# Performance work log

Hardware: AMD Instinct MI355X
Metric: run time of the kernel (lower is better)

## Reference

```python
import jax, jax.numpy as jnp
import numpy as np

N_NODES = 50000
IN_CH = 128
OUT_CH = 64
N_EDGES = 800000
K_HOPS = 2


def setup_inputs() -> dict:
    key = jax.random.key(0)
    k1, k2, k3, k4 = jax.random.split(key, 4)
    x = jax.random.normal(k1, (N_NODES, IN_CH), dtype=jnp.float32)
    edge_index = jax.random.randint(k2, (2, N_EDGES), 0, N_NODES, dtype=jnp.int64)
    # SGC linear layer params (torch Linear default init approx)
    scale = 1.0 / np.sqrt(IN_CH)
    W = jax.random.uniform(k3, (IN_CH, OUT_CH), dtype=jnp.float32, minval=-scale, maxval=scale)
    b = jax.random.uniform(k4, (OUT_CH,), dtype=jnp.float32, minval=-scale, maxval=scale)
    return {"x": x, "edge_index": edge_index, "W": W, "b": b}


def _sgc_propagate(x, row, col, K):
    # GCN symmetric normalization with self-loops: S = D^-1/2 (A+I) D^-1/2
    n = x.shape[0]
    loop = jnp.arange(n, dtype=row.dtype)
    row = jnp.concatenate([row, loop])
    col = jnp.concatenate([col, loop])
    ones = jnp.ones(row.shape[0], dtype=x.dtype)
    deg = jax.ops.segment_sum(ones, col, num_segments=n)
    dinv = jnp.where(deg > 0, jax.lax.rsqrt(deg), 0.0)
    norm = dinv[row] * dinv[col]  # [E+N]
    for _ in range(K):
        # gather source features, weight, scatter-add to targets
        msg = norm[:, None] * x[row]  # [E+N, C]
        x = jax.ops.segment_sum(msg, col, num_segments=n)
    return x


def reference(x, edge_index, W, b):
    # Dropout is identity in eval mode (deterministic reference).
    row, col = edge_index[0], edge_index[1]
    h = _sgc_propagate(x, row, col, K_HOPS)  # [N, IN_CH]
    return h @ W + b  # [N, OUT_CH]
```

## Files before the change

kernel.cpp:

```cpp
#include <hip/hip_runtime.h>

#define N_NODES 50000
#define IN_CH   128
#define OUT_CH  64
#define N_EDGES 800000
#define CAP     96
#define SCAT_B  242
#define GEMM_B  782


__device__ __forceinline__ unsigned int bpack(float a, float b) {
    unsigned int ua = __float_as_uint(a), ub = __float_as_uint(b);
    unsigned int ra = (ua + 0x7fffu + ((ua >> 16) & 1u)) >> 16;
    unsigned int rb = (ub + 0x7fffu + ((ub >> 16) & 1u)) & 0xffff0000u;
    return (ra & 0xffffu) | rb;
}


__global__ __launch_bounds__(256) void gemm_scatter(const float* __restrict__ x,
        const float* __restrict__ W, const int* __restrict__ row,
        const int* __restrict__ col, float* __restrict__ y,
        int* __restrict__ fill, unsigned short* __restrict__ esrc) {
    const int bid = blockIdx.x, tid = threadIdx.x;
    if (bid < SCAT_B) {
        for (int e = bid * 256 + tid; e < N_EDGES; e += SCAT_B * 256) {
            int s = row[e], t = col[e];
            int pos = atomicAdd(&fill[t], 1);
            if (pos < CAP) esrc[pos * N_NODES + t] = (unsigned short)s;
        }
        return;
    }
    __shared__ float sW[IN_CH * OUT_CH];
    {
        const float4* W4 = (const float4*)W;
        float4* sW4 = (float4*)sW;
        #pragma unroll
        for (int i = 0; i < 8; ++i) sW4[tid + i * 256] = W4[tid + i * 256];
    }

    const int q   = tid & 7;
    const int seg = tid >> 3;
    const int n0  = (bid - SCAT_B) * 64;
    const int na  = n0 + seg;
    const int nb  = n0 + 32 + seg;
    const int ca  = (na < N_NODES) ? na : N_NODES - 1;
    const int cb  = (nb < N_NODES) ? nb : N_NODES - 1;

    float xa[16], xb[16];
    {
        const float4* ra = (const float4*)(x + (size_t)ca * IN_CH + q * 16);
        const float4* rb = (const float4*)(x + (size_t)cb * IN_CH + q * 16);
        #pragma unroll
        for (int j = 0; j < 4; ++j) {
            ((float4*)xa)[j] = ra[j];
            ((float4*)xb)[j] = rb[j];
        }
    }
    __syncthreads();

    float acca[8] = {}, accb[8] = {};
    for (int k0 = 0; k0 < 8; ++k0) {
        #pragma unroll
        for (int i = 0; i < 16; ++i) {
            float ka = __shfl(xa[i], k0, 8);
            float kb = __shfl(xb[i], k0, 8);
            const float* wr = &sW[((k0 * 16 + i) << 6) + q * 8];
            float4 w0 = *(const float4*)wr;
            float4 w1 = *(const float4*)(wr + 4);
            acca[0] += ka * w0.x; acca[1] += ka * w0.y;
            acca[2] += ka * w0.z; acca[3] += ka * w0.w;
            acca[4] += ka * w1.x; acca[5] += ka * w1.y;
            acca[6] += ka * w1.z; acca[7] += ka * w1.w;
            accb[0] += kb * w0.x; accb[1] += kb * w0.y;
            accb[2] += kb * w0.z; accb[3] += kb * w0.w;
            accb[4] += kb * w1.x; accb[5] += kb * w1.y;
            accb[6] += kb * w1.z; accb[7] += kb * w1.w;
        }
    }
    if (na < N_NODES) {
        *(float4*)(y + (size_t)na * OUT_CH + q * 8) =
            make_float4(acca[0], acca[1], acca[2], acca[3]);
        *(float4*)(y + (size_t)na * OUT_CH + q * 8 + 4) =
            make_float4(acca[4], acca[5], acca[6], acca[7]);
    }
    if (nb < N_NODES) {
        *(float4*)(y + (size_t)nb * OUT_CH + q * 8) =
            make_float4(accb[0], accb[1], accb[2], accb[3]);
        *(float4*)(y + (size_t)nb * OUT_CH + q * 8 + 4) =
            make_float4(accb[4], accb[5], accb[6], accb[7]);
    }
}


__global__ __launch_bounds__(256) void scale_z0(const float* __restrict__ y,
        const int* __restrict__ fill, uint4* __restrict__ z0) {
    int gid = blockIdx.x * 256 + threadIdx.x;
    if (gid >= N_NODES * 8) return;
    int n = gid >> 3, q = gid & 7;
    int deg = fill[n]; if (deg > CAP) deg = CAP;
    float d = rsqrtf((float)(deg + 1));
    float4 a = ((const float4*)y)[n * 16 + q * 2];
    float4 b = ((const float4*)y)[n * 16 + q * 2 + 1];
    uint4 pk;
    pk.x = bpack(d * a.x, d * a.y);
    pk.y = bpack(d * a.z, d * a.w);
    pk.z = bpack(d * b.x, d * b.y);
    pk.w = bpack(d * b.z, d * b.w);
    z0[gid] = pk;
}


__global__ __launch_bounds__(256) void hop_gather(const uint4* __restrict__ hin,
        void* __restrict__ hout, const int* __restrict__ fill,
        const unsigned short* __restrict__ esrc, const float* __restrict__ bias,
        int last) {
    int lane = threadIdx.x & 63;
    int g = lane >> 3;
    int q = lane & 7;
    int t = __builtin_amdgcn_readfirstlane(blockIdx.x * 4 + (threadIdx.x >> 6));
    if (t >= N_NODES) return;
    int deg = fill[t]; if (deg > CAP) deg = CAP;

    float acc[8] = {};
    if (g == 0) {
        uint4 r = hin[t * 8 + q];
        const unsigned int rw[4] = { r.x, r.y, r.z, r.w };
        #pragma unroll
        for (int j = 0; j < 4; ++j) {
            acc[2 * j]     = __uint_as_float(rw[j] << 16);
            acc[2 * j + 1] = __uint_as_float(rw[j] & 0xffff0000u);
        }
    }
    for (int base = 0; base < deg; base += 8) {
        int e = base + g;
        if (e < deg) {
            int s = (int)esrc[(size_t)e * N_NODES + t];
            uint4 r = hin[s * 8 + q];
            const unsigned int rw[4] = { r.x, r.y, r.z, r.w };
            #pragma unroll
            for (int j = 0; j < 4; ++j) {
                acc[2 * j]     += __uint_as_float(rw[j] << 16);
                acc[2 * j + 1] += __uint_as_float(rw[j] & 0xffff0000u);
            }
        }
    }
    #pragma unroll
    for (int j = 0; j < 8; ++j) {
        acc[j] += __shfl_xor(acc[j], 8);
        acc[j] += __shfl_xor(acc[j], 16);
        acc[j] += __shfl_xor(acc[j], 32);
    }
    if (g == 0) {
        if (!last) {
            float rdeg = 1.0f / (float)(deg + 1);
            uint4 pk;
            pk.x = bpack(acc[0] * rdeg, acc[1] * rdeg);
            pk.y = bpack(acc[2] * rdeg, acc[3] * rdeg);
            pk.z = bpack(acc[4] * rdeg, acc[5] * rdeg);
            pk.w = bpack(acc[6] * rdeg, acc[7] * rdeg);
            ((uint4*)hout)[t * 8 + q] = pk;
        } else {
            float d = rsqrtf((float)(deg + 1));
            float4 b0 = ((const float4*)bias)[q * 2];
            float4 b1 = ((const float4*)bias)[q * 2 + 1];
            float4 o0 = make_float4(d * acc[0] + b0.x, d * acc[1] + b0.y,
                                    d * acc[2] + b0.z, d * acc[3] + b0.w);
            float4 o1 = make_float4(d * acc[4] + b1.x, d * acc[5] + b1.y,
                                    d * acc[6] + b1.z, d * acc[7] + b1.w);
            ((float4*)hout)[t * 16 + q * 2]     = o0;
            ((float4*)hout)[t * 16 + q * 2 + 1] = o1;
        }
    }
}


extern "C" void kernel_launch(void* const* d_in, const int* in_sizes, int n_in,
                              void* d_out, int out_size, void* d_ws, size_t ws_size,
                              hipStream_t stream) {
    const float* x  = (const float*)d_in[0];
    const int*   ei = (const int*)d_in[1];
    const float* W  = (const float*)d_in[2];
    const float* b  = (const float*)d_in[3];
    float*       out = (float*)d_out;

    const int* row = ei;
    const int* col = ei + N_EDGES;

    char* ws = (char*)d_ws;
    size_t a = 0;
    auto alloc = [&](size_t bytes) { char* p = ws + a; a = (a + bytes + 255) & ~(size_t)255; return p; };
    int*            fill = (int*)            alloc(N_NODES * sizeof(int));
    unsigned short* esrc = (unsigned short*) alloc((size_t)CAP * N_NODES * sizeof(unsigned short));
    float*          y    = (float*)          alloc((size_t)N_NODES * OUT_CH * sizeof(float));
    unsigned int*   z0   = (unsigned int*)   alloc((size_t)N_NODES * OUT_CH * 2);
    unsigned int*   z1   = (unsigned int*)   alloc((size_t)N_NODES * OUT_CH * 2);

    hipMemsetAsync(fill, 0, N_NODES * sizeof(int), stream);

    const int B = 256;
    int gS = (N_NODES * 8 + B - 1) / B;
    int gH = (N_NODES + 3) / 4;

    gemm_scatter<<<SCAT_B + GEMM_B, B, 0, stream>>>(x, W, row, col, y, fill, esrc);
    scale_z0<<<gS, B, 0, stream>>>(y, fill, (uint4*)z0);
    hop_gather<<<gH, B, 0, stream>>>((const uint4*)z0, (void*)z1, fill, esrc, b, 0);
    hop_gather<<<gH, B, 0, stream>>>((const uint4*)z1, (void*)out, fill, esrc, b, 1);
}
```

Measured before the change: 169.1 us.

## Partition edge bucketing by target range with shared-memory counters per edge chunk

Replaces global atomic fill counters with blocks that each own a target-node partition and an edge chunk, counting with LDS atomics and writing per-chunk 8-bit fill counts. This removes the memset and the contended global atomics, and splits the GEMM into its own kernel. The cost is that every block reads its whole edge chunk (32x redundant edge reads), the gather loop now walks 8 chunk segments per node, and each chunk is capped at 16 edges, which could drop edges in rare cases.

Measured after the change: 258.9 us. 1.53x slower.

```diff
diff --git a/kernel.cpp b/kernel.cpp
--- a/kernel.cpp
+++ b/kernel.cpp
@@ -4,8 +4,11 @@
 #define IN_CH   128
 #define OUT_CH  64
 #define N_EDGES 800000
-#define CAP     96
-#define SCAT_B  242
+#define P_PART  32
+#define C_CHUNK 8
+#define T_PER_P 1563
+#define E_PER_C 100000
+#define CAP_C   16
 #define GEMM_B  782
 
 
@@ -17,19 +20,46 @@
 }
 
 
-__global__ __launch_bounds__(256) void gemm_scatter(const float* __restrict__ x,
-        const float* __restrict__ W, const int* __restrict__ row,
-        const int* __restrict__ col, float* __restrict__ y,
-        int* __restrict__ fill, unsigned short* __restrict__ esrc) {
-    const int bid = blockIdx.x, tid = threadIdx.x;
-    if (bid < SCAT_B) {
-        for (int e = bid * 256 + tid; e < N_EDGES; e += SCAT_B * 256) {
-            int s = row[e], t = col[e];
-            int pos = atomicAdd(&fill[t], 1);
-            if (pos < CAP) esrc[pos * N_NODES + t] = (unsigned short)s;
-        }
-        return;
-    }
+__global__ __launch_bounds__(256) void scatter_part(const int* __restrict__ row,
+        const int* __restrict__ col, unsigned short* __restrict__ esrc,
+        unsigned char* __restrict__ fill8) {
+    __shared__ int lcnt[T_PER_P];
+    const int p  = blockIdx.x >> 3;
+    const int c  = blockIdx.x & 7;
+    const int t0 = p * T_PER_P;
+    int tsz = N_NODES - t0; if (tsz > T_PER_P) tsz = T_PER_P;
+    for (int i = threadIdx.x; i < T_PER_P; i += 256) lcnt[i] = 0;
+    __syncthreads();
+
+    const int e0 = c * E_PER_C;
+    for (int base = threadIdx.x * 4; base < E_PER_C; base += 256 * 4) {
+        int e = e0 + base;
+        int4 t4 = *(const int4*)&col[e];
+        int4 s4 = *(const int4*)&row[e];
+        const int ts[4] = { t4.x, t4.y, t4.z, t4.w };
+        const int ss[4] = { s4.x, s4.y, s4.z, s4.w };
+        #pragma unroll
+        for (int j = 0; j < 4; ++j) {
+            int tl = ts[j] - t0;
+            if (tl >= 0 && tl < tsz) {
+                int pos = atomicAdd(&lcnt[tl], 1);
+                if (pos < CAP_C)
+                    esrc[(size_t)(c * CAP_C + pos) * N_NODES + ts[j]] =
+                        (unsigned short)ss[j];
+            }
+        }
+    }
+    __syncthreads();
+    for (int i = threadIdx.x; i < tsz; i += 256) {
+        int v = lcnt[i]; if (v > CAP_C) v = CAP_C;
+        fill8[(size_t)c * N_NODES + t0 + i] = (unsigned char)v;
+    }
+}
+
+
+__global__ __launch_bounds__(256) void gemm_x(const float* __restrict__ x,
+        const float* __restrict__ W, float* __restrict__ y) {
+    const int tid = threadIdx.x;
     __shared__ float sW[IN_CH * OUT_CH];
     {
         const float4* W4 = (const float4*)W;
@@ -37,10 +67,9 @@
         #pragma unroll
         for (int i = 0; i < 8; ++i) sW4[tid + i * 256] = W4[tid + i * 256];
     }
-
     const int q   = tid & 7;
     const int seg = tid >> 3;
-    const int n0  = (bid - SCAT_B) * 64;
+    const int n0  = blockIdx.x * 64;
     const int na  = n0 + seg;
     const int nb  = n0 + 32 + seg;
     const int ca  = (na < N_NODES) ? na : N_NODES - 1;
@@ -93,11 +122,13 @@
 
 
 __global__ __launch_bounds__(256) void scale_z0(const float* __restrict__ y,
-        const int* __restrict__ fill, uint4* __restrict__ z0) {
+        const unsigned char* __restrict__ fill8, uint4* __restrict__ z0) {
     int gid = blockIdx.x * 256 + threadIdx.x;
     if (gid >= N_NODES * 8) return;
     int n = gid >> 3, q = gid & 7;
-    int deg = fill[n]; if (deg > CAP) deg = CAP;
+    int deg = 0;
+    #pragma unroll
+    for (int c = 0; c < C_CHUNK; ++c) deg += fill8[(size_t)c * N_NODES + n];
     float d = rsqrtf((float)(deg + 1));
     float4 a = ((const float4*)y)[n * 16 + q * 2];
     float4 b = ((const float4*)y)[n * 16 + q * 2 + 1];
@@ -111,7 +142,7 @@
 
 
 __global__ __launch_bounds__(256) void hop_gather(const uint4* __restrict__ hin,
-        void* __restrict__ hout, const int* __restrict__ fill,
+        void* __restrict__ hout, const unsigned char* __restrict__ fill8,
         const unsigned short* __restrict__ esrc, const float* __restrict__ bias,
         int last) {
     int lane = threadIdx.x & 63;
@@ -119,7 +150,14 @@
     int q = lane & 7;
     int t = __builtin_amdgcn_readfirstlane(blockIdx.x * 4 + (threadIdx.x >> 6));
     if (t >= N_NODES) return;
-    int deg = fill[t]; if (deg > CAP) deg = CAP;
+
+    int dcs[C_CHUNK];
+    int deg = 0;
+    #pragma unroll
+    for (int c = 0; c < C_CHUNK; ++c) {
+        dcs[c] = fill8[(size_t)c * N_NODES + t];
+        deg += dcs[c];
+    }
 
     float acc[8] = {};
     if (g == 0) {
@@ -131,16 +169,20 @@
             acc[2 * j + 1] = __uint_as_float(rw[j] & 0xffff0000u);
         }
     }
-    for (int base = 0; base < deg; base += 8) {
-        int e = base + g;
-        if (e < deg) {
-            int s = (int)esrc[(size_t)e * N_NODES + t];
-            uint4 r = hin[s * 8 + q];
-            const unsigned int rw[4] = { r.x, r.y, r.z, r.w };
-            #pragma unroll
-            for (int j = 0; j < 4; ++j) {
-                acc[2 * j]     += __uint_as_float(rw[j] << 16);
-                acc[2 * j + 1] += __uint_as_float(rw[j] & 0xffff0000u);
+    #pragma unroll
+    for (int c = 0; c < C_CHUNK; ++c) {
+        int dc = dcs[c];
+        for (int base = 0; base < dc; base += 8) {
+            int e = base + g;
+            if (e < dc) {
+                int s = (int)esrc[(size_t)(c * CAP_C + e) * N_NODES + t];
+                uint4 r = hin[s * 8 + q];
+                const unsigned int rw[4] = { r.x, r.y, r.z, r.w };
+                #pragma unroll
+                for (int j = 0; j < 4; ++j) {
+                    acc[2 * j]     += __uint_as_float(rw[j] << 16);
+                    acc[2 * j + 1] += __uint_as_float(rw[j] & 0xffff0000u);
+                }
             }
         }
     }
@@ -189,20 +231,19 @@
     char* ws = (char*)d_ws;
     size_t a = 0;
     auto alloc = [&](size_t bytes) { char* p = ws + a; a = (a + bytes + 255) & ~(size_t)255; return p; };
-    int*            fill = (int*)            alloc(N_NODES * sizeof(int));
-    unsigned short* esrc = (unsigned short*) alloc((size_t)CAP * N_NODES * sizeof(unsigned short));
-    float*          y    = (float*)          alloc((size_t)N_NODES * OUT_CH * sizeof(float));
-    unsigned int*   z0   = (unsigned int*)   alloc((size_t)N_NODES * OUT_CH * 2);
-    unsigned int*   z1   = (unsigned int*)   alloc((size_t)N_NODES * OUT_CH * 2);
-
-    hipMemsetAsync(fill, 0, N_NODES * sizeof(int), stream);
+    unsigned short* esrc  = (unsigned short*)alloc((size_t)C_CHUNK * CAP_C * N_NODES * 2);
+    unsigned char*  fill8 = (unsigned char*) alloc((size_t)C_CHUNK * N_NODES);
+    float*          y     = (float*)         alloc((size_t)N_NODES * OUT_CH * sizeof(float));
+    unsigned int*   z0    = (unsigned int*)  alloc((size_t)N_NODES * OUT_CH * 2);
+    unsigned int*   z1    = (unsigned int*)  alloc((size_t)N_NODES * OUT_CH * 2);
 
     const int B = 256;
     int gS = (N_NODES * 8 + B - 1) / B;
     int gH = (N_NODES + 3) / 4;
 
-    gemm_scatter<<<SCAT_B + GEMM_B, B, 0, stream>>>(x, W, row, col, y, fill, esrc);
-    scale_z0<<<gS, B, 0, stream>>>(y, fill, (uint4*)z0);
-    hop_gather<<<gH, B, 0, stream>>>((const uint4*)z0, (void*)z1, fill, esrc, b, 0);
-    hop_gather<<<gH, B, 0, stream>>>((const uint4*)z1, (void*)out, fill, esrc, b, 1);
-}
+    scatter_part<<<P_PART * C_CHUNK, B, 0, stream>>>(row, col, esrc, fill8);
+    gemm_x<<<GEMM_B, B, 0, stream>>>(x, W, y);
+    scale_z0<<<gS, B, 0, stream>>>(y, fill8, (uint4*)z0);
+    hop_gather<<<gH, B, 0, stream>>>((const uint4*)z0, (void*)z1, fill8, esrc, b, 0);
+    hop_gather<<<gH, B, 0, stream>>>((const uint4*)z1, (void*)out, fill8, esrc, b, 1);
+}
```
